# Optimization experiments

Hardware: AMD Instinct MI355X
Metric: run time of the kernel (lower is better)

Reference implementation:

```python
import jax, jax.numpy as jnp
import numpy as np

N, DIM, H, DH = 2048, 1024, 16, 64
LARGE_NEG = -1e10
LN_EPS = 1e-6  # flax LayerNorm default


def setup_inputs() -> dict:
    key = jax.random.key(0)
    ks = jax.random.split(key, 6)
    x = jax.random.normal(ks[0], (N, DIM), dtype=jnp.float32)
    pos_sin = jax.random.uniform(ks[1], (N - 1, DH // 2), dtype=jnp.float32)
    pos_cos = jax.random.uniform(ks[2], (N - 1, DH // 2), dtype=jnp.float32)
    mask = jax.random.bernoulli(ks[3], 0.9, (N - 1,))
    ln_scale = jnp.ones((DIM,), jnp.float32)
    ln_bias = jnp.zeros((DIM,), jnp.float32)
    w_qkv = jax.random.normal(ks[4], (DIM, 3 * H * DH), jnp.float32) * (DIM ** -0.5)
    w_out = jax.random.normal(ks[5], (H * DH, DIM), jnp.float32) * ((H * DH) ** -0.5)
    b_out = jnp.zeros((DIM,), jnp.float32)
    return {"x": x, "pos_sin": pos_sin, "pos_cos": pos_cos, "mask": mask,
            "ln_scale": ln_scale, "ln_bias": ln_bias,
            "w_qkv": w_qkv, "w_out": w_out, "b_out": b_out}


def _rotate_every_two(t):
    # t: [i, h, d] -> pairwise rotation along d
    x1 = t[:, :, ::2]
    x2 = t[:, :, 1::2]
    return jnp.stack((-x2, x1), axis=-1).reshape(t.shape)


def _apply_rope(t, sin, cos):
    # sin/cos: [i, d/2] -> interleave-repeat to [i, 1, d] (einops 'b n -> b (n j)', j=2)
    sin2 = jnp.repeat(sin, 2, axis=-1)[:, None, :]
    cos2 = jnp.repeat(cos, 2, axis=-1)[:, None, :]
    return t * cos2 + _rotate_every_two(t) * sin2


def reference(x, pos_sin, pos_cos, mask, ln_scale, ln_bias, w_qkv, w_out, b_out):
    n, dim_in = x.shape
    scale = dim_in ** -0.5  # NOTE: full model dim, as in the source

    # LayerNorm over last axis
    mu = jnp.mean(x, axis=-1, keepdims=True)
    var = jnp.mean(jnp.square(x - mu), axis=-1, keepdims=True)
    xn = (x - mu) * jax.lax.rsqrt(var + LN_EPS) * ln_scale + ln_bias

    # QKV projection (no bias)
    qkv = xn @ w_qkv  # [n, 3*h*d]
    q, k, v = jnp.split(qkv, 3, axis=-1)
    q, k, v = (t.reshape(n, H, DH) for t in (q, k, v))

    # Selective RoPE: rotate all positions except the first token
    q = q.at[1:].set(_apply_rope(q[1:], pos_sin, pos_cos))
    k = k.at[1:].set(_apply_rope(k[1:], pos_sin, pos_cos))

    # Head-last similarity [i, j, h]
    sim = jnp.einsum('ihd,jhd->ijh', q, k) * scale

    # Padding mask: prepend True for position 0, broadcast as (1, j, 1)
    pad_mask = jnp.pad(mask, (1, 0), constant_values=True)[None, :, None]

    # Causal mask: triu of an (n-1)x(n-1) block padded with False on row/col 0
    tri = jnp.pad(jnp.ones((n - 1, n - 1), bool), ((1, 0), (1, 0)), constant_values=False)
    causal_mask = jnp.triu(tri, 1)[:, :, None]  # k = j - i + 1 = 1
    full_mask = (~causal_mask) & pad_mask

    sim = jnp.where(full_mask, sim, LARGE_NEG)
    attn = jax.nn.softmax(sim, axis=-2)  # softmax over j (non-last axis)

    out = jnp.einsum('ijh,jhd->ihd', attn, v).reshape(n, H * DH)
    return out @ w_out + b_out
```

## Files before the change

kernel.cpp:

```cpp
#include <hip/hip_runtime.h>
#include <hip/hip_bf16.h>
#include <stdint.h>

typedef __bf16 bf16_t;
typedef __bf16 bf16x8 __attribute__((ext_vector_type(8)));
typedef __bf16 bf16x4 __attribute__((ext_vector_type(4)));
typedef float  f32x4  __attribute__((ext_vector_type(4)));

#define DEV __device__ __forceinline__

static constexpr int NTOK = 2048;
static constexpr int DIM  = 1024;
static constexpr int NH   = 16;
static constexpr int DH   = 64;
static constexpr int QKVN = 3072;
static constexpr int SLOTS_PER_HEAD = 40;
static constexpr int PART_SLOTS = 36;
static constexpr int PART_STRIDE = 17408;
static constexpr float L2E = 1.44269504f;

DEV void gload_lds16(const void* g, void* l) {
  __builtin_amdgcn_global_load_lds(
      (__attribute__((address_space(1))) void*)(g),
      (__attribute__((address_space(3))) void*)(l), 16, 0, 0);
}

DEV float bf2f(bf16_t b) { return (float)b; }

__global__ __launch_bounds__(256) void k_ln_tc(const float* __restrict__ x,
                                               const float* __restrict__ gamma,
                                               const float* __restrict__ beta,
                                               bf16_t* __restrict__ xn,
                                               const float* __restrict__ wsrc,
                                               bf16_t* __restrict__ wdst,
                                               const float* __restrict__ wosrc,
                                               bf16_t* __restrict__ wodst) {
  __shared__ float tile[64][65];
  __shared__ float red[8];
  int b = blockIdx.x;
  if (b < NTOK) {
    const int row = b;
    const int t = threadIdx.x;
    const float4* x4 = reinterpret_cast<const float4*>(x);
    float4 v = x4[(size_t)row * 256 + t];
    float s  = v.x + v.y + v.z + v.w;
    float s2 = v.x * v.x + v.y * v.y + v.z * v.z + v.w * v.w;
#pragma unroll
    for (int o = 1; o < 64; o <<= 1) {
      s  += __shfl_xor(s, o, 64);
      s2 += __shfl_xor(s2, o, 64);
    }
    const int w = t >> 6, lane = t & 63;
    if (lane == 0) { red[w] = s; red[4 + w] = s2; }
    __syncthreads();
    s  = red[0] + red[1] + red[2] + red[3];
    s2 = red[4] + red[5] + red[6] + red[7];
    const float mu  = s * (1.0f / 1024.0f);
    const float var = s2 * (1.0f / 1024.0f) - mu * mu;
    const float inv = rsqrtf(var + 1e-6f);
    const float4 g = reinterpret_cast<const float4*>(gamma)[t];
    const float4 bb = reinterpret_cast<const float4*>(beta)[t];
    bf16x4 o;
    o[0] = (bf16_t)((v.x - mu) * inv * g.x + bb.x);
    o[1] = (bf16_t)((v.y - mu) * inv * g.y + bb.y);
    o[2] = (bf16_t)((v.z - mu) * inv * g.z + bb.z);
    o[3] = (bf16_t)((v.w - mu) * inv * g.w + bb.w);
    *reinterpret_cast<bf16x4*>(xn + (size_t)row * DIM + t * 4) = o;
  } else if (b < NTOK + 768) {
    b -= NTOK;
    const int c0 = (b % 48) * 64;
    const int r0 = (b / 48) * 64;
    const int tx = threadIdx.x & 63;
    const int ty = threadIdx.x >> 6;
#pragma unroll
    for (int i = 0; i < 16; ++i) {
      int r = ty + i * 4;
      tile[r][tx] = wsrc[(size_t)(r0 + r) * 3072 + c0 + tx];
    }
    __syncthreads();
#pragma unroll
    for (int i = 0; i < 16; ++i) {
      int r = ty + i * 4;
      wdst[(size_t)(c0 + r) * 1024 + r0 + tx] = (bf16_t)tile[tx][r];
    }
  } else {
    b -= (NTOK + 768);
    const int c0 = (b & 15) * 64;
    const int r0 = (b >> 4) * 64;
    const int tx = threadIdx.x & 63;
    const int ty = threadIdx.x >> 6;
#pragma unroll
    for (int i = 0; i < 16; ++i) {
      int r = ty + i * 4;
      tile[r][tx] = wosrc[(size_t)(r0 + r) * 1024 + c0 + tx];
    }
    __syncthreads();
#pragma unroll
    for (int i = 0; i < 16; ++i) {
      int r = ty + i * 4;
      wodst[(size_t)(c0 + r) * 1024 + r0 + tx] = (bf16_t)tile[tx][r];
    }
  }
}

template <int F32OUT>
__global__ __launch_bounds__(256) void k_gemm_bt(const bf16_t* __restrict__ A,
                                                 const bf16_t* __restrict__ Bt,
                                                 bf16_t* __restrict__ Cb,
                                                 float* __restrict__ Cf,
                                                 const float* __restrict__ bias,
                                                 int M, int N, int K) {
  __shared__ alignas(16) bf16_t As[2][128 * 32];
  __shared__ alignas(16) bf16_t Bs[2][128 * 32];
  const int tid = threadIdx.x, lane = tid & 63, w = tid >> 6;
  const int bm = blockIdx.x * 128, bn = blockIdx.y * 128;
  const int wr = (w >> 1) * 64, wc = (w & 1) * 64;
  f32x4 acc[4][4];
#pragma unroll
  for (int i = 0; i < 4; ++i)
#pragma unroll
    for (int j = 0; j < 4; ++j) acc[i][j] = f32x4{0.f, 0.f, 0.f, 0.f};

  const int srow  = lane >> 2;
  const int scol8 = (lane & 3) * 8;

#define GSTAGE(KT, BUF)                                                               \
  {                                                                                   \
    _Pragma("unroll") for (int it = 0; it < 2; ++it) {                                \
      int seg = w * 2 + it;                                                           \
      gload_lds16(A + (size_t)(bm + seg * 16 + srow) * K + (KT) + scol8,              \
                  (char*)As + (BUF) * 8192 + seg * 1024 + lane * 16);                 \
      gload_lds16(Bt + (size_t)(bn + seg * 16 + srow) * K + (KT) + scol8,             \
                  (char*)Bs + (BUF) * 8192 + seg * 1024 + lane * 16);                 \
    }                                                                                 \
  }

  GSTAGE(0, 0)
  __syncthreads();
  int buf = 0;
  for (int kt = 0; kt < K; kt += 32, buf ^= 1) {
    if (kt + 32 < K) GSTAGE(kt + 32, buf ^ 1)
    bf16x8 af[4], bfr[4];
#pragma unroll
    for (int i = 0; i < 4; ++i) {
      int mrow = wr + i * 16 + (lane & 15);
      af[i] = *reinterpret_cast<const bf16x8*>((const char*)As + buf * 8192 + mrow * 64 +
                                               (lane >> 4) * 16);
    }
#pragma unroll
    for (int j = 0; j < 4; ++j) {
      int nrow = wc + j * 16 + (lane & 15);
      bfr[j] = *reinterpret_cast<const bf16x8*>((const char*)Bs + buf * 8192 + nrow * 64 +
                                                (lane >> 4) * 16);
    }
#pragma unroll
    for (int i = 0; i < 4; ++i)
#pragma unroll
      for (int j = 0; j < 4; ++j)
        acc[i][j] = __builtin_amdgcn_mfma_f32_16x16x32_bf16(af[i], bfr[j], acc[i][j], 0, 0, 0);
    __syncthreads();
  }
#undef GSTAGE

#pragma unroll
  for (int i = 0; i < 4; ++i)
#pragma unroll
    for (int j = 0; j < 4; ++j)
#pragma unroll
      for (int r = 0; r < 4; ++r) {
        int mm = bm + wr + i * 16 + (lane >> 4) * 4 + r;
        int nn = bn + wc + j * 16 + (lane & 15);
        float val = acc[i][j][r];
        if (F32OUT)
          Cf[(size_t)mm * N + nn] = val + bias[nn];
        else
          Cb[(size_t)mm * N + nn] = (bf16_t)val;
      }
}

template <int F32OUT>
__global__ __launch_bounds__(256) void k_gemm64(const bf16_t* __restrict__ A,
                                                const bf16_t* __restrict__ Bt,
                                                bf16_t* __restrict__ Cb,
                                                float* __restrict__ Cf,
                                                const float* __restrict__ bias,
                                                int M, int N, int K) {
  __shared__ alignas(16) bf16_t As[2][64 * 32];
  __shared__ alignas(16) bf16_t Bs[2][128 * 32];
  const int tid = threadIdx.x, lane = tid & 63, w = tid >> 6;
  const int bm = blockIdx.x * 64, bn = blockIdx.y * 128;
  const int wr = (w >> 1) * 32, wc = (w & 1) * 64;
  f32x4 acc[2][4];
#pragma unroll
  for (int i = 0; i < 2; ++i)
#pragma unroll
    for (int j = 0; j < 4; ++j) acc[i][j] = f32x4{0.f, 0.f, 0.f, 0.f};

  const int srow  = lane >> 2;
  const int scol8 = (lane & 3) * 8;

#define GSTAGE64(KT, BUF)                                                             \
  {                                                                                   \
    _Pragma("unroll") for (int it = 0; it < 3; ++it) {                                \
      int s = w * 3 + it;                                                             \
      if (s < 4)                                                                      \
        gload_lds16(A + (size_t)(bm + s * 16 + srow) * K + (KT) + scol8,              \
                    (char*)As + (BUF) * 4096 + s * 1024 + lane * 16);                 \
      else                                                                            \
        gload_lds16(Bt + (size_t)(bn + (s - 4) * 16 + srow) * K + (KT) + scol8,       \
                    (char*)Bs + (BUF) * 8192 + (s - 4) * 1024 + lane * 16);           \
    }                                                                                 \
  }

  GSTAGE64(0, 0)
  __syncthreads();
  int buf = 0;
  for (int kt = 0; kt < K; kt += 32, buf ^= 1) {
    if (kt + 32 < K) GSTAGE64(kt + 32, buf ^ 1)
    bf16x8 af[2], bfr[4];
#pragma unroll
    for (int i = 0; i < 2; ++i) {
      int mrow = wr + i * 16 + (lane & 15);
      af[i] = *reinterpret_cast<const bf16x8*>((const char*)As + buf * 4096 + mrow * 64 +
                                               (lane >> 4) * 16);
    }
#pragma unroll
    for (int j = 0; j < 4; ++j) {
      int nrow = wc + j * 16 + (lane & 15);
      bfr[j] = *reinterpret_cast<const bf16x8*>((const char*)Bs + buf * 8192 + nrow * 64 +
                                                (lane >> 4) * 16);
    }
#pragma unroll
    for (int i = 0; i < 2; ++i)
#pragma unroll
      for (int j = 0; j < 4; ++j)
        acc[i][j] = __builtin_amdgcn_mfma_f32_16x16x32_bf16(af[i], bfr[j], acc[i][j], 0, 0, 0);
    __syncthreads();
  }
#undef GSTAGE64

#pragma unroll
  for (int i = 0; i < 2; ++i)
#pragma unroll
    for (int j = 0; j < 4; ++j)
#pragma unroll
      for (int r = 0; r < 4; ++r) {
        int mm = bm + wr + i * 16 + (lane >> 4) * 4 + r;
        int nn = bn + wc + j * 16 + (lane & 15);
        float val = acc[i][j][r];
        if (F32OUT)
          Cf[(size_t)mm * N + nn] = val + bias[nn];
        else
          Cb[(size_t)mm * N + nn] = (bf16_t)val;
      }
}

__global__ __launch_bounds__(256) void k_rope_vt(bf16_t* __restrict__ qkv,
                                                 const float* __restrict__ psin,
                                                 const float* __restrict__ pcos,
                                                 bf16_t* __restrict__ Vt) {
  __shared__ bf16_t tile[64][72];
  int b = blockIdx.x;
  if (b < NTOK - 1) {
    const int i = b + 1;
    const int t = threadIdx.x;
#pragma unroll
    for (int itr = 0; itr < 4; ++itr) {
      int pidx = itr * 256 + t;
      int half = pidx >> 9;
      int pp   = pidx & 511;
      int hh = pp >> 5, tt2 = pp & 31;
      size_t off = (size_t)i * QKVN + half * 1024 + hh * 64 + tt2 * 2;
      float sn = psin[(size_t)(i - 1) * 32 + tt2];
      float cs = pcos[(size_t)(i - 1) * 32 + tt2];
      unsigned int u = *reinterpret_cast<const unsigned int*>(qkv + off);
      float x0 = bf2f(__builtin_bit_cast(bf16_t, (unsigned short)(u & 0xffffu)));
      float x1 = bf2f(__builtin_bit_cast(bf16_t, (unsigned short)(u >> 16)));
      const float mul = half ? 1.0f : 0.03125f;
      unsigned short b0 = __builtin_bit_cast(unsigned short, (bf16_t)((x0 * cs - x1 * sn) * mul));
      unsigned short b1 = __builtin_bit_cast(unsigned short, (bf16_t)((x1 * cs + x0 * sn) * mul));
      *reinterpret_cast<unsigned int*>(qkv + off) = (unsigned int)b0 | ((unsigned int)b1 << 16);
    }
  } else {
    b -= (NTOK - 1);
    const int n0 = (b & 31) * 64;
    const int h  = b >> 5;
    const int r  = threadIdx.x >> 2;
    const int cq = threadIdx.x & 3;
    const bf16_t* src = qkv + (size_t)(n0 + r) * QKVN + 2048 + h * DH + cq * 16;
    bf16x8 v0 = *reinterpret_cast<const bf16x8*>(src);
    bf16x8 v1 = *reinterpret_cast<const bf16x8*>(src + 8);
#pragma unroll
    for (int e = 0; e < 8; ++e) { tile[r][cq * 16 + e] = v0[e]; tile[r][cq * 16 + 8 + e] = v1[e]; }
    __syncthreads();
    const int d = r;
    bf16x8 o0, o1;
#pragma unroll
    for (int e = 0; e < 8; ++e) { o0[e] = tile[cq * 16 + e][d]; o1[e] = tile[cq * 16 + 8 + e][d]; }
    bf16_t* dst = Vt + ((size_t)h * DH + d) * NTOK + n0 + cq * 16;
    *reinterpret_cast<bf16x8*>(dst)     = o0;
    *reinterpret_cast<bf16x8*>(dst + 8) = o1;
  }
}

__global__ __launch_bounds__(512) void k_attn_part(const bf16_t* __restrict__ qkv,
                                                   const bf16_t* __restrict__ Vt,
                                                   const int* __restrict__ mask,
                                                   char* __restrict__ part,
                                                   bf16_t* __restrict__ Ob) {
  __shared__ alignas(16) bf16_t Ks[2][64][64];
  __shared__ alignas(16) bf16_t Vs[2][64][64];
  __shared__ alignas(16) bf16_t Ps[8][1024];
  __shared__ unsigned char padc[512];

  const int h = blockIdx.y;

  if (blockIdx.x == SLOTS_PER_HEAD) {
    float* qv   = (float*)Ps;
    float* sbuf = (float*)Ks;
    float* red  = (float*)Vs;
    float* red2 = (float*)Vs + 64;
    const int t = threadIdx.x, lane = t & 63, w8 = t >> 6;
    if (t < 64) qv[t] = (float)qkv[h * DH + t];
    __syncthreads();
    float sm[4];
    float lmax = -1e30f;
#pragma unroll
    for (int p = 0; p < 4; ++p) {
      int j = p * 512 + t;
      const bf16_t* kr = qkv + (size_t)j * QKVN + DIM + h * DH;
      float s = 0.f;
#pragma unroll
      for (int u = 0; u < 8; ++u) {
        bf16x8 kv8 = *reinterpret_cast<const bf16x8*>(kr + u * 8);
#pragma unroll
        for (int e = 0; e < 8; ++e) s += qv[u * 8 + e] * (float)kv8[e];
      }
      bool padj = (j == 0) || (mask[j - 1] != 0);
      s = padj ? s * 0.03125f : -1e30f;
      sm[p] = s;
      lmax = fmaxf(lmax, s);
    }
#pragma unroll
    for (int o = 1; o < 64; o <<= 1) lmax = fmaxf(lmax, __shfl_xor(lmax, o, 64));
    if (lane == 0) red[w8] = lmax;
    __syncthreads();
    float M = red[0];
#pragma unroll
    for (int i = 1; i < 8; ++i) M = fmaxf(M, red[i]);
    __syncthreads();
    float ls = 0.f;
#pragma unroll
    for (int p = 0; p < 4; ++p) {
      float pe = __expf(sm[p] - M);
      sbuf[p * 512 + t] = pe;
      ls += pe;
    }
#pragma unroll
    for (int o = 1; o < 64; o <<= 1) ls += __shfl_xor(ls, o, 64);
    if (lane == 0) red[w8] = ls;
    __syncthreads();
    float L = red[0];
#pragma unroll
    for (int i = 1; i < 8; ++i) L += red[i];

    const int d = t & 63, qr = t >> 6;
    const bf16_t* vr = Vt + ((size_t)h * DH + d) * NTOK + qr * 256;
    float a = 0.f;
#pragma unroll 8
    for (int u = 0; u < 32; ++u) {
      bf16x8 v8 = *reinterpret_cast<const bf16x8*>(vr + u * 8);
#pragma unroll
      for (int e = 0; e < 8; ++e) a += sbuf[qr * 256 + u * 8 + e] * (float)v8[e];
    }
    red2[qr * 64 + d] = a;
    __syncthreads();
    if (t < 64) {
      float o = 0.f;
#pragma unroll
      for (int i = 0; i < 8; ++i) o += red2[i * 64 + t];
      Ob[h * DH + t] = (bf16_t)(o / L);
    }
    return;
  }

  const int slot = (SLOTS_PER_HEAD - 1) - blockIdx.x;
  int g;
  if (slot < 4) g = 0; else if (slot < 12) g = 1; else if (slot < 24) g = 2; else g = 3;
  const int tt = slot - 2 * g * (g + 1);
  const int Q = (g << 2) + tt / (g + 1);
  const int c = tt - (tt / (g + 1)) * (g + 1);
  const int q0 = Q * 128;
  const int kbeg = c * 512;
  const int kvlen = (Q + 1) * 128;
  const int klen = min(512, kvlen - kbeg);
  const int ntiles = klen >> 6;
  const int nch = g + 1;

  const int tid = threadIdx.x, lane = tid & 63, w = tid >> 6;

  for (int jr = tid; jr < klen; jr += 512) {
    int j = kbeg + jr;
    padc[jr] = (j == 0) ? 1 : (unsigned char)(mask[j - 1] != 0);
  }

  const int iw = q0 + w * 16;
  bf16x8 qf[2];
  {
    const bf16_t* qp = qkv + (size_t)(iw + (lane & 15)) * QKVN + h * DH + (lane >> 4) * 8;
    qf[0] = *reinterpret_cast<const bf16x8*>(qp);
    qf[1] = *reinterpret_cast<const bf16x8*>(qp + 32);
  }
  bf16x8 ones;
#pragma unroll
  for (int e = 0; e < 8; ++e) ones[e] = (bf16_t)1.0f;

  float m_run[4], m2[4];
  f32x4 acc[4], accl;
#pragma unroll
  for (int r = 0; r < 4; ++r) { m_run[r] = -1e30f; m2[r] = -1e30f; }
#pragma unroll
  for (int df = 0; df < 4; ++df) acc[df] = f32x4{0.f, 0.f, 0.f, 0.f};
  accl = f32x4{0.f, 0.f, 0.f, 0.f};

  const int r8 = lane >> 3;
  const int sw = (lane & 7) ^ r8;

#define STAGE(KB, BUF)                                                                   \
  {                                                                                      \
    _Pragma("unroll") for (int i2 = 0; i2 < 2; ++i2) {                                   \
      int s = w * 2 + i2;                                                                \
      if (s < 8) {                                                                       \
        int row = s * 8 + r8;                                                            \
        gload_lds16(qkv + (size_t)((KB) + row) * QKVN + DIM + h * DH + sw * 8,           \
                    (char*)Ks + (BUF)*8192 + s * 1024 + lane * 16);                      \
      } else {                                                                           \
        int row = (s - 8) * 8 + r8;                                                      \
        gload_lds16(Vt + ((size_t)h * DH + row) * NTOK + (KB) + sw * 8,                  \
                    (char*)Vs + (BUF)*8192 + (s - 8) * 1024 + lane * 16);                \
      }                                                                                  \
    }                                                                                    \
  }

  STAGE(kbeg, 0)

  for (int it = 0; it < ntiles; ++it) {
    const int buf = it & 1;
    if (it + 1 < ntiles) {
      STAGE(kbeg + (it + 1) * 64, buf ^ 1)
      asm volatile("s_waitcnt vmcnt(2)" ::: "memory");
    } else {
      asm volatile("s_waitcnt vmcnt(0)" ::: "memory");
    }
    __builtin_amdgcn_s_barrier();

    const int k0 = kbeg + it * 64;
    if (k0 <= iw + 15) {
      const char* KsT = (const char*)Ks + buf * 8192;
      const char* VsT = (const char*)Vs + buf * 8192;

      f32x4 sfr[4];
      __builtin_amdgcn_s_setprio(1);
#pragma unroll
      for (int jf = 0; jf < 4; ++jf) {
        f32x4 s = f32x4{0.f, 0.f, 0.f, 0.f};
        int jl = jf * 16 + (lane & 15);
#pragma unroll
        for (int ks = 0; ks < 2; ++ks) {
          int inrow = (ks * 64 + (lane >> 4) * 16) ^ ((jl & 7) << 4);
          bf16x8 kf = *reinterpret_cast<const bf16x8*>(KsT + jl * 128 + inrow);
          s = __builtin_amdgcn_mfma_f32_16x16x32_bf16(qf[ks], kf, s, 0, 0, 0);
        }
        sfr[jf] = s;
      }
      __builtin_amdgcn_s_setprio(0);

      float pmax[4] = {-3e38f, -3e38f, -3e38f, -3e38f};
#pragma unroll
      for (int jf = 0; jf < 4; ++jf)
#pragma unroll
        for (int r = 0; r < 4; ++r) pmax[r] = fmaxf(pmax[r], sfr[jf][r]);

      int dok = (pmax[0] <= m_run[0] + 8.f) && (pmax[1] <= m_run[1] + 8.f) &&
                (pmax[2] <= m_run[2] + 8.f) && (pmax[3] <= m_run[3] + 8.f);
      if (!__all(dok)) {
#pragma unroll
        for (int o = 1; o < 16; o <<= 1)
#pragma unroll
          for (int r = 0; r < 4; ++r) pmax[r] = fmaxf(pmax[r], __shfl_xor(pmax[r], o, 64));
#pragma unroll
        for (int r = 0; r < 4; ++r) {
          float mnew = fmaxf(m_run[r], pmax[r]);
          float corr = __builtin_amdgcn_exp2f((m_run[r] - mnew) * L2E);
          m_run[r] = mnew;
          m2[r] = mnew * L2E;
          accl[r] *= corr;
#pragma unroll
          for (int df = 0; df < 4; ++df) acc[df][r] *= corr;
        }
      }

      const bool needC = (k0 + 63 > iw);
#pragma unroll
      for (int jf = 0; jf < 4; ++jf) {
        int jl = jf * 16 + (lane & 15);
        int j = k0 + jl;
        bool padj = padc[j - kbeg] != 0;
#pragma unroll
        for (int r = 0; r < 4; ++r) {
          float pe = __builtin_amdgcn_exp2f(__builtin_fmaf(sfr[jf][r], L2E, -m2[r]));
          bool ok = padj;
          if (needC) ok = ok && (j <= iw + (lane >> 4) * 4 + r);
          pe = ok ? pe : 0.f;
          int m = (lane >> 4) * 4 + r;
          *reinterpret_cast<bf16_t*>((char*)&Ps[w][0] + m * 128 + ((jl * 2) ^ ((m & 7) << 4))) =
              (bf16_t)pe;
        }
      }

      __builtin_amdgcn_s_setprio(1);
#pragma unroll
      for (int ks = 0; ks < 2; ++ks) {
        int mm = lane & 15;
        int inrow = (ks * 64 + (lane >> 4) * 16) ^ ((mm & 7) << 4);
        bf16x8 pa = *reinterpret_cast<const bf16x8*>((const char*)&Ps[w][0] + mm * 128 + inrow);
        accl = __builtin_amdgcn_mfma_f32_16x16x32_bf16(pa, ones, accl, 0, 0, 0);
#pragma unroll
        for (int df = 0; df < 4; ++df) {
          int d = df * 16 + (lane & 15);
          int vin = (ks * 64 + (lane >> 4) * 16) ^ ((d & 7) << 4);
          bf16x8 vf = *reinterpret_cast<const bf16x8*>(VsT + d * 128 + vin);
          acc[df] = __builtin_amdgcn_mfma_f32_16x16x32_bf16(pa, vf, acc[df], 0, 0, 0);
        }
      }
      __builtin_amdgcn_s_setprio(0);
    }
    __builtin_amdgcn_s_barrier();
  }
#undef STAGE

  if (nch == 1) {
#pragma unroll
    for (int r = 0; r < 4; ++r) {
      float inv = 1.0f / accl[r];
      int row = w * 16 + (lane >> 4) * 4 + r;
#pragma unroll
      for (int df = 0; df < 4; ++df) {
        if (q0 + row != 0)
          Ob[(size_t)(q0 + row) * DIM + h * DH + df * 16 + (lane & 15)] =
              (bf16_t)(acc[df][r] * inv);
      }
    }
  } else {
    char* pb = part + (size_t)(h * PART_SLOTS + (slot - 4)) * PART_STRIDE;
    bf16_t* po = (bf16_t*)pb;
    float* pm = (float*)(pb + 16384);
    float* pl = (float*)(pb + 16896);
#pragma unroll
    for (int df = 0; df < 4; ++df)
#pragma unroll
      for (int r = 0; r < 4; ++r) {
        int row = w * 16 + (lane >> 4) * 4 + r;
        po[row * 64 + df * 16 + (lane & 15)] = (bf16_t)acc[df][r];
      }
    if ((lane & 15) == 0) {
#pragma unroll
      for (int r = 0; r < 4; ++r) {
        int row = w * 16 + (lane >> 4) * 4 + r;
        pm[row] = m2[r];
        pl[row] = accl[r];
      }
    }
  }
}

__global__ __launch_bounds__(256) void k_merge(const char* __restrict__ part,
                                               bf16_t* __restrict__ Ob) {
  const int Q = blockIdx.x + 4, h = blockIdx.y;
  const int g = Q >> 2, nch = g + 1;
  const int cum = 2 * g * (g + 1) + (Q & 3) * nch - 4;
  const int t = threadIdx.x;
  const int row = t >> 1, half = t & 1;

  float acc[32];
#pragma unroll
  for (int e = 0; e < 32; ++e) acc[e] = 0.f;
  float M = -3e38f, L = 0.f;

  for (int c = 0; c < nch; ++c) {
    const char* pb = part + (size_t)(h * PART_SLOTS + cum + c) * PART_STRIDE;
    float mc = ((const float*)(pb + 16384))[row];
    float lc = ((const float*)(pb + 16896))[row];
    float Mn = fmaxf(M, mc);
    float sOld = __builtin_amdgcn_exp2f(M - Mn), sNew = __builtin_amdgcn_exp2f(mc - Mn);
    M = Mn;
    L = L * sOld + lc * sNew;
    const bf16_t* od = (const bf16_t*)pb + row * 64 + half * 32;
#pragma unroll
    for (int e4 = 0; e4 < 4; ++e4) {
      bf16x8 o8 = *reinterpret_cast<const bf16x8*>(od + e4 * 8);
#pragma unroll
      for (int e = 0; e < 8; ++e)
        acc[e4 * 8 + e] = acc[e4 * 8 + e] * sOld + (float)o8[e] * sNew;
    }
  }
  const float inv = 1.0f / L;
  bf16_t* dst = Ob + (size_t)(Q * 128 + row) * DIM + h * DH + half * 32;
#pragma unroll
  for (int e4 = 0; e4 < 4; ++e4) {
    bf16x8 r8o;
#pragma unroll
    for (int e = 0; e < 8; ++e) r8o[e] = (bf16_t)(acc[e4 * 8 + e] * inv);
    *reinterpret_cast<bf16x8*>(dst + e4 * 8) = r8o;
  }
}

extern "C" void kernel_launch(void* const* d_in, const int* in_sizes, int n_in,
                              void* d_out, int out_size, void* d_ws, size_t ws_size,
                              hipStream_t stream) {
  const float* x       = (const float*)d_in[0];
  const float* pos_sin = (const float*)d_in[1];
  const float* pos_cos = (const float*)d_in[2];
  const int*   mask    = (const int*)d_in[3];
  const float* ln_s    = (const float*)d_in[4];
  const float* ln_b    = (const float*)d_in[5];
  const float* w_qkv   = (const float*)d_in[6];
  const float* w_out   = (const float*)d_in[7];
  const float* b_out   = (const float*)d_in[8];
  float* out = (float*)d_out;

  if (ws_size < 33554432u) return;

  char* ws = (char*)d_ws;
  bf16_t* qkv  = (bf16_t*)(ws + 0);
  bf16_t* Vt   = (bf16_t*)(ws + 12582912);
  bf16_t* Ob   = (bf16_t*)(ws + 16777216);
  bf16_t* Wot  = (bf16_t*)(ws + 20971520);
  bf16_t* xn   = (bf16_t*)(ws + 23068672);
  bf16_t* Wqt  = (bf16_t*)(ws + 27262976);
  char*   part = ws + 23068672;

  k_ln_tc<<<NTOK + 768 + 256, 256, 0, stream>>>(x, ln_s, ln_b, xn, w_qkv, Wqt, w_out, Wot);
  k_gemm_bt<0><<<dim3(16, 24), 256, 0, stream>>>(xn, Wqt, qkv, nullptr, nullptr,
                                                 NTOK, QKVN, DIM);
  k_rope_vt<<<(NTOK - 1) + 512, 256, 0, stream>>>(qkv, pos_sin, pos_cos, Vt);
  k_attn_part<<<dim3(SLOTS_PER_HEAD + 1, NH), 512, 0, stream>>>(qkv, Vt, mask, part, Ob);
  k_merge<<<dim3(12, 16), 256, 0, stream>>>(part, Ob);
  k_gemm64<1><<<dim3(32, 8), 256, 0, stream>>>(Ob, Wot, nullptr, out, b_out,
                                               NTOK, DIM, DIM);
}
```

Before: 105.7 us.

## Fuse RoPE and V transpose into QKV GEMM epilogue; keep P in registers in attention

The QKV projection GEMM now uses 64x128 tiles and applies RoPE plus the 1/32 Q scaling in its epilogue, pairing adjacent columns with a lane shuffle. It also writes V directly in transposed layout, which removes the separate rope/transpose kernel and its round trip over the QKV buffer. In the attention kernel, S is computed as K·Q^T so the probability fragments land in registers already in the layout the PV MFMA needs. This drops the per-wave LDS P buffer, uses a single running max per lane, and changes the K/V LDS swizzle. The costs are scattered narrow Vt stores, per-element sin/cos loads in the GEMM epilogue, and extra shuffles to broadcast the correction factors.

```diff
diff --git a/kernel.cpp b/kernel.cpp
--- a/kernel.cpp
+++ b/kernel.cpp
@@ -103,48 +103,50 @@
   }
 }
 
-template <int F32OUT>
-__global__ __launch_bounds__(256) void k_gemm_bt(const bf16_t* __restrict__ A,
-                                                 const bf16_t* __restrict__ Bt,
-                                                 bf16_t* __restrict__ Cb,
-                                                 float* __restrict__ Cf,
-                                                 const float* __restrict__ bias,
-                                                 int M, int N, int K) {
-  __shared__ alignas(16) bf16_t As[2][128 * 32];
+__global__ __launch_bounds__(256) void k_gemm_qkv(const bf16_t* __restrict__ A,
+                                                  const bf16_t* __restrict__ Bt,
+                                                  bf16_t* __restrict__ qkv,
+                                                  bf16_t* __restrict__ Vt,
+                                                  const float* __restrict__ psin,
+                                                  const float* __restrict__ pcos) {
+  __shared__ alignas(16) bf16_t As[2][64 * 32];
   __shared__ alignas(16) bf16_t Bs[2][128 * 32];
+  const int K = DIM;
   const int tid = threadIdx.x, lane = tid & 63, w = tid >> 6;
-  const int bm = blockIdx.x * 128, bn = blockIdx.y * 128;
-  const int wr = (w >> 1) * 64, wc = (w & 1) * 64;
-  f32x4 acc[4][4];
-#pragma unroll
-  for (int i = 0; i < 4; ++i)
+  const int bm = blockIdx.x * 64, bn = blockIdx.y * 128;
+  const int wr = (w >> 1) * 32, wc = (w & 1) * 64;
+  f32x4 acc[2][4];
+#pragma unroll
+  for (int i = 0; i < 2; ++i)
 #pragma unroll
     for (int j = 0; j < 4; ++j) acc[i][j] = f32x4{0.f, 0.f, 0.f, 0.f};
 
   const int srow  = lane >> 2;
   const int scol8 = (lane & 3) * 8;
 
-#define GSTAGE(KT, BUF)                                                               \
+#define GSTAGEQ(KT, BUF)                                                              \
   {                                                                                   \
-    _Pragma("unroll") for (int it = 0; it < 2; ++it) {                                \
-      int seg = w * 2 + it;                                                           \
-      gload_lds16(A + (size_t)(bm + seg * 16 + srow) * K + (KT) + scol8,              \
-                  (char*)As + (BUF) * 8192 + seg * 1024 + lane * 16);                 \
-      gload_lds16(Bt + (size_t)(bn + seg * 16 + srow) * K + (KT) + scol8,             \
-                  (char*)Bs + (BUF) * 8192 + seg * 1024 + lane * 16);                 \
+    _Pragma("unroll") for (int it = 0; it < 3; ++it) {                                \
+      int s = w * 3 + it;                                                             \
+      if (s < 4)                                                                      \
+        gload_lds16(A + (size_t)(bm + s * 16 + srow) * K + (KT) + scol8,              \
+                    (char*)As + (BUF) * 4096 + s * 1024 + lane * 16);                 \
+      else                                                                            \
+        gload_lds16(Bt + (size_t)(bn + (s - 4) * 16 + srow) * K + (KT) + scol8,       \
+                    (char*)Bs + (BUF) * 8192 + (s - 4) * 1024 + lane * 16);           \
     }                                                                                 \
   }
 
-  GSTAGE(0, 0)
+  GSTAGEQ(0, 0)
   __syncthreads();
   int buf = 0;
   for (int kt = 0; kt < K; kt += 32, buf ^= 1) {
-    if (kt + 32 < K) GSTAGE(kt + 32, buf ^ 1)
-    bf16x8 af[4], bfr[4];
-#pragma unroll
-    for (int i = 0; i < 4; ++i) {
+    if (kt + 32 < K) GSTAGEQ(kt + 32, buf ^ 1)
+    bf16x8 af[2], bfr[4];
+#pragma unroll
+    for (int i = 0; i < 2; ++i) {
       int mrow = wr + i * 16 + (lane & 15);
-      af[i] = *reinterpret_cast<const bf16x8*>((const char*)As + buf * 8192 + mrow * 64 +
+      af[i] = *reinterpret_cast<const bf16x8*>((const char*)As + buf * 4096 + mrow * 64 +
                                                (lane >> 4) * 16);
     }
 #pragma unroll
@@ -154,28 +156,48 @@
                                                 (lane >> 4) * 16);
     }
 #pragma unroll
-    for (int i = 0; i < 4; ++i)
+    for (int i = 0; i < 2; ++i)
 #pragma unroll
       for (int j = 0; j < 4; ++j)
         acc[i][j] = __builtin_amdgcn_mfma_f32_16x16x32_bf16(af[i], bfr[j], acc[i][j], 0, 0, 0);
     __syncthreads();
   }
-#undef GSTAGE
-
-#pragma unroll
-  for (int i = 0; i < 4; ++i)
-#pragma unroll
-    for (int j = 0; j < 4; ++j)
-#pragma unroll
-      for (int r = 0; r < 4; ++r) {
-        int mm = bm + wr + i * 16 + (lane >> 4) * 4 + r;
+#undef GSTAGEQ
+
+  if (bn >= 2048) {
+#pragma unroll
+    for (int i = 0; i < 2; ++i)
+#pragma unroll
+      for (int j = 0; j < 4; ++j) {
+        int d = bn - 2048 + wc + j * 16 + (lane & 15);
+        int n0v = bm + wr + i * 16 + (lane >> 4) * 4;
+        bf16x4 v4;
+#pragma unroll
+        for (int r = 0; r < 4; ++r) v4[r] = (bf16_t)acc[i][j][r];
+        *reinterpret_cast<bf16x4*>(Vt + (size_t)d * NTOK + n0v) = v4;
+      }
+  } else {
+#pragma unroll
+    for (int i = 0; i < 2; ++i)
+#pragma unroll
+      for (int j = 0; j < 4; ++j) {
         int nn = bn + wc + j * 16 + (lane & 15);
-        float val = acc[i][j][r];
-        if (F32OUT)
-          Cf[(size_t)mm * N + nn] = val + bias[nn];
-        else
-          Cb[(size_t)mm * N + nn] = (bf16_t)val;
-      }
+        int tt = (nn & 63) >> 1;
+        bool isq = nn < 1024;
+#pragma unroll
+        for (int r = 0; r < 4; ++r) {
+          int mm = bm + wr + i * 16 + (lane >> 4) * 4 + r;
+          float v = acc[i][j][r];
+          float p = __shfl_xor(v, 1, 64);
+          int pidx = (mm >= 1 ? mm - 1 : 0) * 32 + tt;
+          float sn = psin[pidx], cs = pcos[pidx];
+          float roped = (nn & 1) ? (v * cs + p * sn) : (v * cs - p * sn);
+          if (mm < 1) roped = v;
+          if (isq && mm >= 1) roped *= 0.03125f;
+          qkv[(size_t)mm * QKVN + nn] = (bf16_t)roped;
+        }
+      }
+  }
 }
 
 template <int F32OUT>
@@ -255,54 +277,6 @@
       }
 }
 
-__global__ __launch_bounds__(256) void k_rope_vt(bf16_t* __restrict__ qkv,
-                                                 const float* __restrict__ psin,
-                                                 const float* __restrict__ pcos,
-                                                 bf16_t* __restrict__ Vt) {
-  __shared__ bf16_t tile[64][72];
-  int b = blockIdx.x;
-  if (b < NTOK - 1) {
-    const int i = b + 1;
-    const int t = threadIdx.x;
-#pragma unroll
-    for (int itr = 0; itr < 4; ++itr) {
-      int pidx = itr * 256 + t;
-      int half = pidx >> 9;
-      int pp   = pidx & 511;
-      int hh = pp >> 5, tt2 = pp & 31;
-      size_t off = (size_t)i * QKVN + half * 1024 + hh * 64 + tt2 * 2;
-      float sn = psin[(size_t)(i - 1) * 32 + tt2];
-      float cs = pcos[(size_t)(i - 1) * 32 + tt2];
-      unsigned int u = *reinterpret_cast<const unsigned int*>(qkv + off);
-      float x0 = bf2f(__builtin_bit_cast(bf16_t, (unsigned short)(u & 0xffffu)));
-      float x1 = bf2f(__builtin_bit_cast(bf16_t, (unsigned short)(u >> 16)));
-      const float mul = half ? 1.0f : 0.03125f;
-      unsigned short b0 = __builtin_bit_cast(unsigned short, (bf16_t)((x0 * cs - x1 * sn) * mul));
-      unsigned short b1 = __builtin_bit_cast(unsigned short, (bf16_t)((x1 * cs + x0 * sn) * mul));
-      *reinterpret_cast<unsigned int*>(qkv + off) = (unsigned int)b0 | ((unsigned int)b1 << 16);
-    }
-  } else {
-    b -= (NTOK - 1);
-    const int n0 = (b & 31) * 64;
-    const int h  = b >> 5;
-    const int r  = threadIdx.x >> 2;
-    const int cq = threadIdx.x & 3;
-    const bf16_t* src = qkv + (size_t)(n0 + r) * QKVN + 2048 + h * DH + cq * 16;
-    bf16x8 v0 = *reinterpret_cast<const bf16x8*>(src);
-    bf16x8 v1 = *reinterpret_cast<const bf16x8*>(src + 8);
-#pragma unroll
-    for (int e = 0; e < 8; ++e) { tile[r][cq * 16 + e] = v0[e]; tile[r][cq * 16 + 8 + e] = v1[e]; }
-    __syncthreads();
-    const int d = r;
-    bf16x8 o0, o1;
-#pragma unroll
-    for (int e = 0; e < 8; ++e) { o0[e] = tile[cq * 16 + e][d]; o1[e] = tile[cq * 16 + 8 + e][d]; }
-    bf16_t* dst = Vt + ((size_t)h * DH + d) * NTOK + n0 + cq * 16;
-    *reinterpret_cast<bf16x8*>(dst)     = o0;
-    *reinterpret_cast<bf16x8*>(dst + 8) = o1;
-  }
-}
-
 __global__ __launch_bounds__(512) void k_attn_part(const bf16_t* __restrict__ qkv,
                                                    const bf16_t* __restrict__ Vt,
                                                    const int* __restrict__ mask,
@@ -310,13 +284,12 @@
                                                    bf16_t* __restrict__ Ob) {
   __shared__ alignas(16) bf16_t Ks[2][64][64];
   __shared__ alignas(16) bf16_t Vs[2][64][64];
-  __shared__ alignas(16) bf16_t Ps[8][1024];
-  __shared__ unsigned char padc[512];
+  __shared__ alignas(16) float padf[512];
 
   const int h = blockIdx.y;
 
   if (blockIdx.x == SLOTS_PER_HEAD) {
-    float* qv   = (float*)Ps;
+    float* qv   = padf;
     float* sbuf = (float*)Ks;
     float* red  = (float*)Vs;
     float* red2 = (float*)Vs + 64;
@@ -385,29 +358,31 @@
   }
 
   const int slot = (SLOTS_PER_HEAD - 1) - blockIdx.x;
-  int g;
-  if (slot < 4) g = 0; else if (slot < 12) g = 1; else if (slot < 24) g = 2; else g = 3;
-  const int tt = slot - 2 * g * (g + 1);
-  const int Q = (g << 2) + tt / (g + 1);
-  const int c = tt - (tt / (g + 1)) * (g + 1);
+  int gq;
+  if (slot < 4) gq = 0; else if (slot < 12) gq = 1; else if (slot < 24) gq = 2; else gq = 3;
+  const int tt = slot - 2 * gq * (gq + 1);
+  const int Q = (gq << 2) + tt / (gq + 1);
+  const int c2 = tt - (tt / (gq + 1)) * (gq + 1);
   const int q0 = Q * 128;
-  const int kbeg = c * 512;
+  const int kbeg = c2 * 512;
   const int kvlen = (Q + 1) * 128;
   const int klen = min(512, kvlen - kbeg);
   const int ntiles = klen >> 6;
-  const int nch = g + 1;
+  const int nch = gq + 1;
 
   const int tid = threadIdx.x, lane = tid & 63, w = tid >> 6;
+  const int g = lane >> 4;
+  const int c = lane & 15;
 
   for (int jr = tid; jr < klen; jr += 512) {
     int j = kbeg + jr;
-    padc[jr] = (j == 0) ? 1 : (unsigned char)(mask[j - 1] != 0);
+    padf[jr] = (j == 0 || mask[j - 1] != 0) ? 1.f : 0.f;
   }
 
   const int iw = q0 + w * 16;
   bf16x8 qf[2];
   {
-    const bf16_t* qp = qkv + (size_t)(iw + (lane & 15)) * QKVN + h * DH + (lane >> 4) * 8;
+    const bf16_t* qp = qkv + (size_t)(iw + c) * QKVN + h * DH + g * 8;
     qf[0] = *reinterpret_cast<const bf16x8*>(qp);
     qf[1] = *reinterpret_cast<const bf16x8*>(qp + 32);
   }
@@ -415,21 +390,19 @@
 #pragma unroll
   for (int e = 0; e < 8; ++e) ones[e] = (bf16_t)1.0f;
 
-  float m_run[4], m2[4];
+  float m_run = -1e30f, m2 = -1e30f;
   f32x4 acc[4], accl;
-#pragma unroll
-  for (int r = 0; r < 4; ++r) { m_run[r] = -1e30f; m2[r] = -1e30f; }
 #pragma unroll
   for (int df = 0; df < 4; ++df) acc[df] = f32x4{0.f, 0.f, 0.f, 0.f};
   accl = f32x4{0.f, 0.f, 0.f, 0.f};
 
   const int r8 = lane >> 3;
-  const int sw = (lane & 7) ^ r8;
 
 #define STAGE(KB, BUF)                                                                   \
   {                                                                                      \
     _Pragma("unroll") for (int i2 = 0; i2 < 2; ++i2) {                                   \
       int s = w * 2 + i2;                                                                \
+      int sw = (lane & 7) ^ r8 ^ ((s & 3) << 1);                                         \
       if (s < 8) {                                                                       \
         int row = s * 8 + r8;                                                            \
         gload_lds16(qkv + (size_t)((KB) + row) * QKVN + DIM + h * DH + sw * 8,           \
@@ -462,75 +435,68 @@
       f32x4 sfr[4];
       __builtin_amdgcn_s_setprio(1);
 #pragma unroll
-      for (int jf = 0; jf < 4; ++jf) {
+      for (int f = 0; f < 4; ++f) {
+        int key7 = ((f & 1) * 4) | (c & 3);
+        int key = (f >> 1) * 32 + (c >> 2) * 8 + key7;
+        int phi = key7 ^ (((c >> 2) & 3) << 1);
         f32x4 s = f32x4{0.f, 0.f, 0.f, 0.f};
-        int jl = jf * 16 + (lane & 15);
-#pragma unroll
-        for (int ks = 0; ks < 2; ++ks) {
-          int inrow = (ks * 64 + (lane >> 4) * 16) ^ ((jl & 7) << 4);
-          bf16x8 kf = *reinterpret_cast<const bf16x8*>(KsT + jl * 128 + inrow);
-          s = __builtin_amdgcn_mfma_f32_16x16x32_bf16(qf[ks], kf, s, 0, 0, 0);
+#pragma unroll
+        for (int kd = 0; kd < 2; ++kd) {
+          bf16x8 kf = *reinterpret_cast<const bf16x8*>(
+              KsT + key * 128 + (((kd * 4 + g) ^ phi) << 4));
+          s = __builtin_amdgcn_mfma_f32_16x16x32_bf16(kf, qf[kd], s, 0, 0, 0);
         }
-        sfr[jf] = s;
+        sfr[f] = s;
       }
       __builtin_amdgcn_s_setprio(0);
 
-      float pmax[4] = {-3e38f, -3e38f, -3e38f, -3e38f};
-#pragma unroll
-      for (int jf = 0; jf < 4; ++jf)
-#pragma unroll
-        for (int r = 0; r < 4; ++r) pmax[r] = fmaxf(pmax[r], sfr[jf][r]);
-
-      int dok = (pmax[0] <= m_run[0] + 8.f) && (pmax[1] <= m_run[1] + 8.f) &&
-                (pmax[2] <= m_run[2] + 8.f) && (pmax[3] <= m_run[3] + 8.f);
-      if (!__all(dok)) {
-#pragma unroll
-        for (int o = 1; o < 16; o <<= 1)
-#pragma unroll
-          for (int r = 0; r < 4; ++r) pmax[r] = fmaxf(pmax[r], __shfl_xor(pmax[r], o, 64));
+      float pm = fmaxf(fmaxf(sfr[0][0], sfr[0][1]), fmaxf(sfr[0][2], sfr[0][3]));
+#pragma unroll
+      for (int f = 1; f < 4; ++f)
+        pm = fmaxf(pm, fmaxf(fmaxf(sfr[f][0], sfr[f][1]), fmaxf(sfr[f][2], sfr[f][3])));
+      pm = fmaxf(pm, __shfl_xor(pm, 16, 64));
+      pm = fmaxf(pm, __shfl_xor(pm, 32, 64));
+
+      if (!__all(pm <= m_run + 8.f)) {
+        float mnew = fmaxf(m_run, pm);
+        float corr = __builtin_amdgcn_exp2f((m_run - mnew) * L2E);
+        m_run = mnew;
+        m2 = mnew * L2E;
 #pragma unroll
         for (int r = 0; r < 4; ++r) {
-          float mnew = fmaxf(m_run[r], pmax[r]);
-          float corr = __builtin_amdgcn_exp2f((m_run[r] - mnew) * L2E);
-          m_run[r] = mnew;
-          m2[r] = mnew * L2E;
-          accl[r] *= corr;
-#pragma unroll
-          for (int df = 0; df < 4; ++df) acc[df][r] *= corr;
+          float cr = __shfl(corr, g * 4 + r, 64);
+          accl[r] *= cr;
+#pragma unroll
+          for (int df = 0; df < 4; ++df) acc[df][r] *= cr;
         }
       }
 
       const bool needC = (k0 + 63 > iw);
-#pragma unroll
-      for (int jf = 0; jf < 4; ++jf) {
-        int jl = jf * 16 + (lane & 15);
-        int j = k0 + jl;
-        bool padj = padc[j - kbeg] != 0;
+      const int qlane = iw + c;
+      bf16x8 pa[2];
+#pragma unroll
+      for (int f = 0; f < 4; ++f) {
+        int jb = (k0 - kbeg) + (f >> 1) * 32 + g * 8 + (f & 1) * 4;
+        f32x4 pad4 = *reinterpret_cast<const f32x4*>(padf + jb);
 #pragma unroll
         for (int r = 0; r < 4; ++r) {
-          float pe = __builtin_amdgcn_exp2f(__builtin_fmaf(sfr[jf][r], L2E, -m2[r]));
-          bool ok = padj;
-          if (needC) ok = ok && (j <= iw + (lane >> 4) * 4 + r);
-          pe = ok ? pe : 0.f;
-          int m = (lane >> 4) * 4 + r;
-          *reinterpret_cast<bf16_t*>((char*)&Ps[w][0] + m * 128 + ((jl * 2) ^ ((m & 7) << 4))) =
-              (bf16_t)pe;
+          float pe = __builtin_amdgcn_exp2f(__builtin_fmaf(sfr[f][r], L2E, -m2)) * pad4[r];
+          if (needC) pe = (kbeg + jb + r <= qlane) ? pe : 0.f;
+          pa[f >> 1][(f & 1) * 4 + r] = (bf16_t)pe;
         }
       }
 
       __builtin_amdgcn_s_setprio(1);
 #pragma unroll
       for (int ks = 0; ks < 2; ++ks) {
-        int mm = lane & 15;
-        int inrow = (ks * 64 + (lane >> 4) * 16) ^ ((mm & 7) << 4);
-        bf16x8 pa = *reinterpret_cast<const bf16x8*>((const char*)&Ps[w][0] + mm * 128 + inrow);
-        accl = __builtin_amdgcn_mfma_f32_16x16x32_bf16(pa, ones, accl, 0, 0, 0);
+        accl = __builtin_amdgcn_mfma_f32_16x16x32_bf16(pa[ks], ones, accl, 0, 0, 0);
 #pragma unroll
         for (int df = 0; df < 4; ++df) {
-          int d = df * 16 + (lane & 15);
-          int vin = (ks * 64 + (lane >> 4) * 16) ^ ((d & 7) << 4);
-          bf16x8 vf = *reinterpret_cast<const bf16x8*>(VsT + d * 128 + vin);
-          acc[df] = __builtin_amdgcn_mfma_f32_16x16x32_bf16(pa, vf, acc[df], 0, 0, 0);
+          int d = df * 16 + c;
+          int phv = (d & 7) ^ (((d >> 3) & 3) << 1);
+          bf16x8 vf = *reinterpret_cast<const bf16x8*>(
+              VsT + d * 128 + (((ks * 4 + g) ^ phv) << 4));
+          acc[df] = __builtin_amdgcn_mfma_f32_16x16x32_bf16(pa[ks], vf, acc[df], 0, 0, 0);
         }
       }
       __builtin_amdgcn_s_setprio(0);
@@ -543,32 +509,34 @@
 #pragma unroll
     for (int r = 0; r < 4; ++r) {
       float inv = 1.0f / accl[r];
-      int row = w * 16 + (lane >> 4) * 4 + r;
+      int row = w * 16 + g * 4 + r;
 #pragma unroll
       for (int df = 0; df < 4; ++df) {
         if (q0 + row != 0)
-          Ob[(size_t)(q0 + row) * DIM + h * DH + df * 16 + (lane & 15)] =
-              (bf16_t)(acc[df][r] * inv);
+          Ob[(size_t)(q0 + row) * DIM + h * DH + df * 16 + c] = (bf16_t)(acc[df][r] * inv);
       }
     }
   } else {
     char* pb = part + (size_t)(h * PART_SLOTS + (slot - 4)) * PART_STRIDE;
     bf16_t* po = (bf16_t*)pb;
-    float* pm = (float*)(pb + 16384);
-    float* pl = (float*)(pb + 16896);
+    float* pmo = (float*)(pb + 16384);
+    float* plo = (float*)(pb + 16896);
+    float mq[4];
+#pragma unroll
+    for (int r = 0; r < 4; ++r) mq[r] = __shfl(m2, g * 4 + r, 64);
 #pragma unroll
     for (int df = 0; df < 4; ++df)
 #pragma unroll
       for (int r = 0; r < 4; ++r) {
-        int row = w * 16 + (lane >> 4) * 4 + r;
-        po[row * 64 + df * 16 + (lane & 15)] = (bf16_t)acc[df][r];
-      }
-    if ((lane & 15) == 0) {
+        int row = w * 16 + g * 4 + r;
+        po[row * 64 + df * 16 + c] = (bf16_t)acc[df][r];
+      }
+    if (c == 0) {
 #pragma unroll
       for (int r = 0; r < 4; ++r) {
-        int row = w * 16 + (lane >> 4) * 4 + r;
-        pm[row] = m2[r];
-        pl[row] = accl[r];
+        int row = w * 16 + g * 4 + r;
+        pmo[row] = mq[r];
+        plo[row] = accl[r];
       }
     }
   }
@@ -641,9 +609,7 @@
   char*   part = ws + 23068672;
 
   k_ln_tc<<<NTOK + 768 + 256, 256, 0, stream>>>(x, ln_s, ln_b, xn, w_qkv, Wqt, w_out, Wot);
-  k_gemm_bt<0><<<dim3(16, 24), 256, 0, stream>>>(xn, Wqt, qkv, nullptr, nullptr,
-                                                 NTOK, QKVN, DIM);
-  k_rope_vt<<<(NTOK - 1) + 512, 256, 0, stream>>>(qkv, pos_sin, pos_cos, Vt);
+  k_gemm_qkv<<<dim3(32, 24), 256, 0, stream>>>(xn, Wqt, qkv, Vt, pos_sin, pos_cos);
   k_attn_part<<<dim3(SLOTS_PER_HEAD + 1, NH), 512, 0, stream>>>(qkv, Vt, mask, part, Ob);
   k_merge<<<dim3(12, 16), 256, 0, stream>>>(part, Ob);
   k_gemm64<1><<<dim3(32, 8), 256, 0, stream>>>(Ob, Wot, nullptr, out, b_out,
```

New measurement: 96.99 us. -8.2%, faster.
